# Performance work log

Hardware: AMD Instinct MI355X
Metric: run time of the kernel (lower is better)

Reference implementation:

```python
import jax, jax.numpy as jnp
import numpy as np

B, S, D, H, M = 2, 2048, 1024, 16, 4096  # batch, seqlen, dim, n_heads, max_seq_len
HD = D // H  # head_dim = 64
EPS = 1e-5


def layernorm(x, g, b):
    mu = jnp.mean(x, axis=-1, keepdims=True)
    var = jnp.mean((x - mu) ** 2, axis=-1, keepdims=True)
    return (x - mu) * jax.lax.rsqrt(var + EPS) * g + b


def setup_inputs() -> dict:
    key = jax.random.key(0)
    ks = jax.random.split(key, 5)
    x = jax.random.normal(ks[0], (B, S, D), jnp.float32)
    # causal mask: >=0 -> keep, negative -> drop (forward does att *= mask >= 0)
    i = jnp.arange(S)
    mask = jnp.where(i[None, :] <= i[:, None], 0, -1).astype(jnp.int32)[None, None]
    w1 = jax.random.normal(ks[1], (4 * D, D), jnp.float32) * (D ** -0.5)
    b1 = jnp.zeros((4 * D,), jnp.float32)
    w2 = jax.random.normal(ks[2], (D, D), jnp.float32) * (D ** -0.5)
    b2 = jnp.zeros((D,), jnp.float32)
    g1 = jnp.ones((D,), jnp.float32)
    beta1 = jnp.zeros((D,), jnp.float32)
    g2 = jnp.ones((D,), jnp.float32)
    beta2 = jnp.zeros((D,), jnp.float32)
    pos_w = jax.random.normal(ks[3], (2 * M - 1,), jnp.float32) * 0.02
    return dict(x=x, mask=mask, w1=w1, b1=b1, w2=w2, b2=b2,
                g1=g1, beta1=beta1, g2=g2, beta2=beta2, pos_w=pos_w)


def reference(x, mask, w1, b1, w2, b2, g1, beta1, g2, beta2, pos_w):
    # f1 + silu, split into gate u and q/k/v
    h = jax.nn.silu(x @ w1.T + b1)                      # [B,S,4D]
    u, q, k, v = jnp.split(h, 4, axis=-1)
    to_heads = lambda t: t.reshape(B, S, H, HD).transpose(0, 2, 1, 3)  # [B,H,S,HD]
    u, q, k, v = map(to_heads, (u, q, k, v))
    # relative positional bias: bias[i,j] = pos_w[M-1 + (j - i)]
    rel = jnp.arange(S)[None, :] - jnp.arange(S)[:, None]
    bias = pos_w[M - 1 + rel]                           # [S,S]
    att = jax.nn.silu(jnp.einsum('bhqd,bhkd->bhqk', q, k) + bias)
    att = att * (mask >= 0)                             # [B,H,S,S]
    y = jnp.einsum('bhqk,bhkd->bhqd', att, v) * u
    y = y.transpose(0, 2, 1, 3).reshape(B, S, D)
    y = layernorm(y, g1, beta1)
    y = y @ w2.T + b2
    return layernorm(y + x, g2, beta2)
```

## Files before the change

### kernel.cpp

```cpp
#include <hip/hip_runtime.h>
#include <hip/hip_bf16.h>

#define BN   2
#define SEQ  2048
#define DIM  1024
#define NH   16
#define HD   64
#define D4   4096
#define MAXS 4096

using bf16 = __hip_bfloat16;
typedef __bf16 bf16x8 __attribute__((ext_vector_type(8)));
typedef float  f32x4  __attribute__((ext_vector_type(4)));

__device__ __forceinline__ float bf2f(bf16 v){ return __bfloat162float(v); }
__device__ __forceinline__ bf16  f2bf(float v){ return __float2bfloat16(v); }
__device__ __forceinline__ float silu_f(float v){
  const float e = __expf(-v);
  return v * __builtin_amdgcn_rcpf(1.f + e);
}

__device__ __forceinline__ void async16(void* lds, const void* g){
  __builtin_amdgcn_global_load_lds((const __attribute__((address_space(1))) void*)g,
                                   (__attribute__((address_space(3))) void*)lds, 16, 0, 0);
}
__device__ __forceinline__ f32x4 mfma16(bf16x8 a, bf16x8 b, f32x4 c){
  return __builtin_amdgcn_mfma_f32_16x16x32_bf16(a, b, c, 0, 0, 0);
}

__global__ __launch_bounds__(256) void f2bk3(
    const float* __restrict__ a, bf16* __restrict__ ao, int na,
    const float* __restrict__ b, bf16* __restrict__ bo, int nb,
    const float* __restrict__ c, bf16* __restrict__ co)
{
  int i = (blockIdx.x * 256 + threadIdx.x) * 4;
  const float* in; bf16* out;
  if (i < na){ in = a; out = ao; }
  else if (i < na + nb){ in = b; out = bo; i -= na; }
  else { in = c; out = co; i -= na + nb; }
  const float4 v = *(const float4*)(in + i);
  bf16 t0 = f2bf(v.x), t1 = f2bf(v.y), t2 = f2bf(v.z), t3 = f2bf(v.w);
  ushort4 o;
  o.x = *(unsigned short*)&t0; o.y = *(unsigned short*)&t1;
  o.z = *(unsigned short*)&t2; o.w = *(unsigned short*)&t3;
  *(ushort4*)((unsigned short*)out + i) = o;
}

template<int NTOT>
__global__ __launch_bounds__(256) void gemm_bt(
    const bf16* __restrict__ A, const bf16* __restrict__ W,
    const float* __restrict__ bias, bf16* __restrict__ outb, bf16* __restrict__ vt)
{
  constexpr int K = DIM;
  const int ntiles = NTOT / 128;
  const int m0 = (int)(blockIdx.x / ntiles) * 128;
  const int n0 = (int)(blockIdx.x % ntiles) * 128;
  __shared__ bf16 Al[128*32];
  __shared__ bf16 Bl[128*32];
  const int tid = threadIdx.x, wave = tid>>6, lane = tid&63;
  const int quad = lane>>4, l16 = lane&15;
  const int srow = lane>>2;
  const int sg   = ((lane&3) ^ ((lane>>3)&3)) * 8;
  const int wm = (wave>>1)*64, wn = (wave&1)*64;
  const int rkey = ((l16>>1)&3);

  f32x4 acc[4][4];
  #pragma unroll
  for (int i=0;i<4;i++)
    #pragma unroll
    for (int j=0;j<4;j++) acc[i][j] = (f32x4){0.f,0.f,0.f,0.f};

  const bf16* aB = A + m0*K;
  const bf16* wB = W + n0*K;

  for (int k0 = 0; k0 < K; k0 += 32){
    async16(&Al[wave*1024      ], aB + (wave*32      + srow)*K + k0 + sg);
    async16(&Al[wave*1024 + 512], aB + (wave*32 + 16 + srow)*K + k0 + sg);
    async16(&Bl[wave*1024      ], wB + (wave*32      + srow)*K + k0 + sg);
    async16(&Bl[wave*1024 + 512], wB + (wave*32 + 16 + srow)*K + k0 + sg);
    __syncthreads();
    bf16x8 af[4], bv[4];
    #pragma unroll
    for (int mt=0;mt<4;mt++) af[mt] = *(const bf16x8*)&Al[(wm+mt*16+l16)*32 + (quad ^ rkey)*8];
    #pragma unroll
    for (int nt=0;nt<4;nt++) bv[nt] = *(const bf16x8*)&Bl[(wn+nt*16+l16)*32 + (quad ^ rkey)*8];
    #pragma unroll
    for (int mt=0;mt<4;mt++)
      #pragma unroll
      for (int nt=0;nt<4;nt++)
        acc[mt][nt] = mfma16(af[mt], bv[nt], acc[mt][nt]);
    __syncthreads();
  }

  const bool vtile = (NTOT == 4096) && (n0 >= 3*DIM);
  if (!vtile){
    #pragma unroll
    for (int mt=0;mt<4;mt++){
      #pragma unroll
      for (int nt=0;nt<4;nt++){
        const int row = m0 + wm + mt*16 + quad*4;
        const int col = n0 + wn + nt*16 + l16;
        const float bvv = bias[col];
        #pragma unroll
        for (int r=0;r<4;r++){
          float v = silu_f(acc[mt][nt][r] + bvv);
          outb[(row+r)*NTOT + col] = f2bf(v);
        }
      }
    }
  } else {
    #pragma unroll
    for (int mt=0;mt<4;mt++){
      #pragma unroll
      for (int nt=0;nt<4;nt++){
        const int row = m0 + wm + mt*16 + quad*4;
        const int colg = n0 + wn + nt*16 + l16;
        const float bvv = bias[colg];
        const int col = colg - 3*DIM;
        const int hh = col >> 6, d = col & 63;
        const int bb = row >> 11, sl = row & 2047;
        ushort4 o;
        float v0 = silu_f(acc[mt][nt][0] + bvv);
        float v1 = silu_f(acc[mt][nt][1] + bvv);
        float v2 = silu_f(acc[mt][nt][2] + bvv);
        float v3 = silu_f(acc[mt][nt][3] + bvv);
        bf16 t0=f2bf(v0), t1=f2bf(v1), t2=f2bf(v2), t3=f2bf(v3);
        o.x=*(unsigned short*)&t0; o.y=*(unsigned short*)&t1;
        o.z=*(unsigned short*)&t2; o.w=*(unsigned short*)&t3;
        *(ushort4*)&vt[((bb*NH + hh)*HD + d)*SEQ + sl] = o;
      }
    }
  }
}

__global__ __launch_bounds__(256) void gemm_bt2(
    const bf16* __restrict__ A, const bf16* __restrict__ W,
    const float* __restrict__ bias, const float* __restrict__ resid,
    float* __restrict__ outf)
{
  constexpr int K = DIM, NTOT = DIM;
  const int ntiles = NTOT / 64;
  const int m0 = (int)(blockIdx.x / ntiles) * 128;
  const int n0 = (int)(blockIdx.x % ntiles) * 64;
  __shared__ bf16 Al[128*32];
  __shared__ bf16 Bl[64*32];
  const int tid = threadIdx.x, wave = tid>>6, lane = tid&63;
  const int quad = lane>>4, l16 = lane&15;
  const int srow = lane>>2;
  const int sg   = ((lane&3) ^ ((lane>>3)&3)) * 8;
  const int wm = wave*32;
  const int rkey = ((l16>>1)&3);

  f32x4 acc[2][4];
  #pragma unroll
  for (int i=0;i<2;i++)
    #pragma unroll
    for (int j=0;j<4;j++) acc[i][j] = (f32x4){0.f,0.f,0.f,0.f};

  const bf16* aB = A + m0*K;
  const bf16* wB = W + n0*K;

  for (int k0 = 0; k0 < K; k0 += 32){
    async16(&Al[wave*1024      ], aB + (wave*32      + srow)*K + k0 + sg);
    async16(&Al[wave*1024 + 512], aB + (wave*32 + 16 + srow)*K + k0 + sg);
    async16(&Bl[wave*512       ], wB + (wave*16      + srow)*K + k0 + sg);
    __syncthreads();
    bf16x8 af[2], bv[4];
    #pragma unroll
    for (int mt=0;mt<2;mt++) af[mt] = *(const bf16x8*)&Al[(wm+mt*16+l16)*32 + (quad ^ rkey)*8];
    #pragma unroll
    for (int nt=0;nt<4;nt++) bv[nt] = *(const bf16x8*)&Bl[(nt*16+l16)*32 + (quad ^ rkey)*8];
    #pragma unroll
    for (int mt=0;mt<2;mt++)
      #pragma unroll
      for (int nt=0;nt<4;nt++)
        acc[mt][nt] = mfma16(af[mt], bv[nt], acc[mt][nt]);
    __syncthreads();
  }

  #pragma unroll
  for (int mt=0;mt<2;mt++){
    #pragma unroll
    for (int nt=0;nt<4;nt++){
      const int row = m0 + wm + mt*16 + quad*4;
      const int col = n0 + nt*16 + l16;
      const float bvv = bias[col];
      #pragma unroll
      for (int r=0;r<4;r++){
        outf[(row+r)*NTOT + col] = acc[mt][nt][r] + bvv + resid[(row+r)*NTOT + col];
      }
    }
  }
}

__global__ __launch_bounds__(256) void attn(
    const bf16* __restrict__ h, const bf16* __restrict__ vt,
    const float* __restrict__ pw, bf16* __restrict__ y)
{
  const int bid = blockIdx.x;
  const int g  = (bid & 7) + ((bid >> 7) << 3);
  const int qp = (bid >> 3) & 15;
  const int hh = g & 15, b = g >> 4;
  __shared__ bf16 Kl[128*64];
  __shared__ bf16 Vl[64*128];
  __shared__ bf16 Pl[4][16*136];
  __shared__ float pwl[256];
  const int tid = threadIdx.x, wave = tid>>6, lane = tid&63;
  const int quad = lane>>4, l16 = lane&15;

  const bf16* kgb = h + b*SEQ*D4 + 2*DIM + hh*HD;
  const bf16* vgb = vt + (b*NH + hh)*HD*SEQ;
  const int krow8 = lane>>3;
  const int kgo   = ((lane&7) ^ krow8) * 8;
  const int vrow4 = lane>>4;

  #pragma unroll
  for (int pass = 0; pass < 2; ++pass){
    const int qt = pass ? (31 - qp) : qp;
    const int q0 = qt * 64;

    const bf16* qbase = h + (b*SEQ + q0 + wave*16 + l16)*D4 + DIM + hh*HD;
    bf16x8 qf[2];
    qf[0] = *(const bf16x8*)(qbase + quad*8);
    qf[1] = *(const bf16x8*)(qbase + 32 + quad*8);

    f32x4 oacc[4];
    #pragma unroll
    for (int nt=0;nt<4;nt++) oacc[nt] = (f32x4){0.f,0.f,0.f,0.f};

    const int kmax = q0 + 64;

    bf16x8 kreg[4], vreg[4];
    float pv;
    #pragma unroll
    for (int t=0;t<4;t++)
      kreg[t] = *(const bf16x8*)(kgb + (wave*32 + t*8 + krow8)*D4 + kgo);
    #pragma unroll
    for (int t=0;t<4;t++){
      const int vg = ((lane&15) ^ (t*4 + vrow4)) * 8;
      vreg[t] = *(const bf16x8*)(vgb + (wave*16 + t*4 + vrow4)*SEQ + vg);
    }
    pv = pw[MAXS - 1 - q0 - 63 + tid];

    for (int k0 = 0; k0 < kmax; k0 += 128){
      __syncthreads();
      #pragma unroll
      for (int t=0;t<4;t++)
        *(bf16x8*)&Kl[(wave*32 + t*8)*64 + lane*8] = kreg[t];
      #pragma unroll
      for (int t=0;t<4;t++)
        *(bf16x8*)&Vl[(wave*16 + t*4)*128 + lane*8] = vreg[t];
      pwl[tid] = pv;
      __syncthreads();

      if (k0 + 128 < kmax){
        const int kn = k0 + 128;
        #pragma unroll
        for (int t=0;t<4;t++)
          kreg[t] = *(const bf16x8*)(kgb + (kn + wave*32 + t*8 + krow8)*D4 + kgo);
        #pragma unroll
        for (int t=0;t<4;t++){
          const int vg = ((lane&15) ^ (t*4 + vrow4)) * 8;
          vreg[t] = *(const bf16x8*)(vgb + (wave*16 + t*4 + vrow4)*SEQ + kn + vg);
        }
        pv = pw[MAXS - 1 + kn - q0 - 63 + tid];
      }

      f32x4 sacc[8];
      #pragma unroll
      for (int nt=0;nt<8;nt++) sacc[nt] = (f32x4){0.f,0.f,0.f,0.f};
      __builtin_amdgcn_s_setprio(1);
      #pragma unroll
      for (int ks=0;ks<2;ks++){
        #pragma unroll
        for (int nt=0;nt<8;nt++){
          bf16x8 kf = *(const bf16x8*)&Kl[(nt*16 + l16)*64 + ((ks*4 + quad) ^ (l16&7))*8];
          sacc[nt] = mfma16(kf, qf[ks], sacc[nt]);
        }
      }
      __builtin_amdgcn_s_setprio(0);

      const int dq = q0 - k0;
      const int qrl = wave*16 + l16;
      #pragma unroll
      for (int nt=0;nt<8;nt++){
        const int kb = nt*16 + quad*4;
        ushort4 o;
        bf16 tb[4];
        #pragma unroll
        for (int r=0;r<4;r++){
          const int d = kb + r - qrl;
          const float bias = pwl[d + 63];
          const float sv = silu_f(sacc[nt][r] + bias);
          tb[r] = f2bf((d <= dq) ? sv : 0.f);
        }
        o.x=*(unsigned short*)&tb[0]; o.y=*(unsigned short*)&tb[1];
        o.z=*(unsigned short*)&tb[2]; o.w=*(unsigned short*)&tb[3];
        *(ushort4*)&Pl[wave][l16*136 + kb] = o;
      }

      __builtin_amdgcn_s_setprio(1);
      #pragma unroll
      for (int ks=0;ks<4;ks++){
        bf16x8 pf = *(const bf16x8*)&Pl[wave][l16*136 + ks*32 + quad*8];
        #pragma unroll
        for (int nt=0;nt<4;nt++){
          bf16x8 vf = *(const bf16x8*)&Vl[(nt*16 + l16)*128 + ((ks*4 + quad) ^ l16)*8];
          oacc[nt] = mfma16(pf, vf, oacc[nt]);
        }
      }
      __builtin_amdgcn_s_setprio(0);
    }

    const int qrow = q0 + wave*16 + quad*4;
    #pragma unroll
    for (int nt=0;nt<4;nt++){
      const int c = hh*HD + nt*16 + l16;
      #pragma unroll
      for (int r=0;r<4;r++){
        const int srow = b*SEQ + qrow + r;
        const float uu = bf2f(h[srow*D4 + c]);
        y[srow*DIM + c] = f2bf(oacc[nt][r] * uu);
      }
    }
    __syncthreads();
  }
}


template<bool FP32IN, bool FP32OUT>
__global__ __launch_bounds__(256) void lnorm(const void* __restrict__ in,
    const float* __restrict__ g, const float* __restrict__ be, void* __restrict__ out)
{
  const int row = blockIdx.x;
  const int tid = threadIdx.x, wave = tid>>6, lane = tid&63;
  const int c0 = tid*4;
  float v[4];
  if (FP32IN){
    const float* p = (const float*)in + row*DIM + c0;
    #pragma unroll
    for (int j=0;j<4;j++) v[j] = p[j];
  } else {
    const bf16* p = (const bf16*)in + row*DIM + c0;
    #pragma unroll
    for (int j=0;j<4;j++) v[j] = bf2f(p[j]);
  }
  float s = 0.f, ss = 0.f;
  #pragma unroll
  for (int j=0;j<4;j++){ s += v[j]; ss += v[j]*v[j]; }
  #pragma unroll
  for (int off=32; off>0; off>>=1){
    s  += __shfl_down(s, off);
    ss += __shfl_down(ss, off);
  }
  __shared__ float red[8];
  if (lane==0){ red[wave] = s; red[4+wave] = ss; }
  __syncthreads();
  s  = red[0]+red[1]+red[2]+red[3];
  ss = red[4]+red[5]+red[6]+red[7];
  const float mu   = s * (1.f/DIM);
  const float var  = ss * (1.f/DIM) - mu*mu;
  const float rstd = rsqrtf(var + 1e-5f);
  #pragma unroll
  for (int j=0;j<4;j++){
    const int c = c0 + j;
    const float o = (v[j]-mu)*rstd*g[c] + be[c];
    if (FP32OUT) ((float*)out)[row*DIM + c] = o;
    else         ((bf16*)out)[row*DIM + c] = f2bf(o);
  }
}

extern "C" void kernel_launch(void* const* d_in, const int* in_sizes, int n_in,
                              void* d_out, int out_size, void* d_ws, size_t ws_size,
                              hipStream_t stream)
{
  const float* x   = (const float*)d_in[0];
  const float* w1  = (const float*)d_in[2];
  const float* b1  = (const float*)d_in[3];
  const float* w2  = (const float*)d_in[4];
  const float* b2  = (const float*)d_in[5];
  const float* g1  = (const float*)d_in[6];
  const float* be1 = (const float*)d_in[7];
  const float* g2  = (const float*)d_in[8];
  const float* be2 = (const float*)d_in[9];
  const float* pw  = (const float*)d_in[10];

  char* ws = (char*)d_ws;
  bf16*  h   = (bf16*)(ws);
  bf16*  vt  = (bf16*)(ws + (32u<<20));
  bf16*  y   = (bf16*)(ws + (40u<<20));
  bf16*  xb  = (bf16*)(ws + (48u<<20));
  bf16*  w1b = (bf16*)(ws + (56u<<20));
  bf16*  w2b = (bf16*)(ws + (64u<<20));
  bf16*  l1  = (bf16*)(ws + (66u<<20));
  float* z   = (float*)(ws + (74u<<20));

  const int NX  = BN*SEQ*DIM;
  const int NW1 = 4*DIM*DIM;
  const int NW2 = DIM*DIM;
  f2bk3<<<dim3((NX+NW1+NW2)/1024), dim3(256), 0, stream>>>(x, xb, NX, w1, w1b, NW1, w2, w2b);

  gemm_bt<4096><<<dim3(1024), dim3(256), 0, stream>>>(xb, w1b, b1, h, vt);
  attn<<<dim3(512), dim3(256), 0, stream>>>(h, vt, pw, y);
  lnorm<false,false><<<dim3(4096), dim3(256), 0, stream>>>(y, g1, be1, l1);
  gemm_bt2<<<dim3(512), dim3(256), 0, stream>>>(l1, w2b, b2, x, z);
  lnorm<true,true><<<dim3(4096), dim3(256), 0, stream>>>(z, g2, be2, d_out);
}
```

Baseline: 241.7 us.

## Split attention into one query tile per block, alias P over K in LDS

The attention kernel now launches 1024 blocks with one 64-row query tile each, replacing 512 blocks that each handled a balanced pair of tiles. Block order is reversed so the heaviest causal tiles start first. The P scratch buffer now shares LDS with the K tile, separated by an extra barrier, which shrinks LDS use so launch_bounds can ask for 4 blocks per CU. Tiles lying fully below the diagonal skip the mask select. The cost is an extra sync per k-step and reliance on the hardware scheduler to balance the uneven per-block work.

```diff
diff --git a/kernel.cpp b/kernel.cpp
--- a/kernel.cpp
+++ b/kernel.cpp
@@ -193,18 +193,21 @@
   }
 }
 
-__global__ __launch_bounds__(256) void attn(
+__global__ __launch_bounds__(256, 4) void attn(
     const bf16* __restrict__ h, const bf16* __restrict__ vt,
     const float* __restrict__ pw, bf16* __restrict__ y)
 {
   const int bid = blockIdx.x;
-  const int g  = (bid & 7) + ((bid >> 7) << 3);
-  const int qp = (bid >> 3) & 15;
+  const int g  = (bid & 7) + ((bid >> 8) << 3);
+  const int qt = 31 - ((bid >> 3) & 31);
   const int hh = g & 15, b = g >> 4;
-  __shared__ bf16 Kl[128*64];
-  __shared__ bf16 Vl[64*128];
-  __shared__ bf16 Pl[4][16*136];
-  __shared__ float pwl[256];
+
+  __shared__ __align__(16) char smem[17408 + 16384 + 1024];
+  bf16*  Kl  = (bf16*)smem;
+  bf16*  Pl  = (bf16*)smem;
+  bf16*  Vl  = (bf16*)(smem + 17408);
+  float* pwl = (float*)(smem + 17408 + 16384);
+
   const int tid = threadIdx.x, wave = tid>>6, lane = tid&63;
   const int quad = lane>>4, l16 = lane&15;
 
@@ -214,79 +217,93 @@
   const int kgo   = ((lane&7) ^ krow8) * 8;
   const int vrow4 = lane>>4;
 
-  #pragma unroll
-  for (int pass = 0; pass < 2; ++pass){
-    const int qt = pass ? (31 - qp) : qp;
-    const int q0 = qt * 64;
-
-    const bf16* qbase = h + (b*SEQ + q0 + wave*16 + l16)*D4 + DIM + hh*HD;
-    bf16x8 qf[2];
-    qf[0] = *(const bf16x8*)(qbase + quad*8);
-    qf[1] = *(const bf16x8*)(qbase + 32 + quad*8);
-
-    f32x4 oacc[4];
-    #pragma unroll
-    for (int nt=0;nt<4;nt++) oacc[nt] = (f32x4){0.f,0.f,0.f,0.f};
-
-    const int kmax = q0 + 64;
-
-    bf16x8 kreg[4], vreg[4];
-    float pv;
+  const int q0 = qt * 64;
+
+  const bf16* qbase = h + (b*SEQ + q0 + wave*16 + l16)*D4 + DIM + hh*HD;
+  bf16x8 qf[2];
+  qf[0] = *(const bf16x8*)(qbase + quad*8);
+  qf[1] = *(const bf16x8*)(qbase + 32 + quad*8);
+
+  f32x4 oacc[4];
+  #pragma unroll
+  for (int nt=0;nt<4;nt++) oacc[nt] = (f32x4){0.f,0.f,0.f,0.f};
+
+  const int kmax = q0 + 64;
+
+  bf16x8 kreg[4], vreg[4];
+  float pv;
+  #pragma unroll
+  for (int t=0;t<4;t++)
+    kreg[t] = *(const bf16x8*)(kgb + (wave*32 + t*8 + krow8)*D4 + kgo);
+  #pragma unroll
+  for (int t=0;t<4;t++){
+    const int vg = ((lane&15) ^ (t*4 + vrow4)) * 8;
+    vreg[t] = *(const bf16x8*)(vgb + (wave*16 + t*4 + vrow4)*SEQ + vg);
+  }
+  pv = pw[MAXS - 1 - q0 - 63 + tid];
+
+  for (int k0 = 0; k0 < kmax; k0 += 128){
+    __syncthreads();
     #pragma unroll
     for (int t=0;t<4;t++)
-      kreg[t] = *(const bf16x8*)(kgb + (wave*32 + t*8 + krow8)*D4 + kgo);
-    #pragma unroll
-    for (int t=0;t<4;t++){
-      const int vg = ((lane&15) ^ (t*4 + vrow4)) * 8;
-      vreg[t] = *(const bf16x8*)(vgb + (wave*16 + t*4 + vrow4)*SEQ + vg);
-    }
-    pv = pw[MAXS - 1 - q0 - 63 + tid];
-
-    for (int k0 = 0; k0 < kmax; k0 += 128){
-      __syncthreads();
+      *(bf16x8*)&Kl[(wave*32 + t*8)*64 + lane*8] = kreg[t];
+    #pragma unroll
+    for (int t=0;t<4;t++)
+      *(bf16x8*)&Vl[(wave*16 + t*4)*128 + lane*8] = vreg[t];
+    pwl[tid] = pv;
+    __syncthreads();
+
+    if (k0 + 128 < kmax){
+      const int kn = k0 + 128;
       #pragma unroll
       for (int t=0;t<4;t++)
-        *(bf16x8*)&Kl[(wave*32 + t*8)*64 + lane*8] = kreg[t];
-      #pragma unroll
-      for (int t=0;t<4;t++)
-        *(bf16x8*)&Vl[(wave*16 + t*4)*128 + lane*8] = vreg[t];
-      pwl[tid] = pv;
-      __syncthreads();
-
-      if (k0 + 128 < kmax){
-        const int kn = k0 + 128;
-        #pragma unroll
-        for (int t=0;t<4;t++)
-          kreg[t] = *(const bf16x8*)(kgb + (kn + wave*32 + t*8 + krow8)*D4 + kgo);
-        #pragma unroll
-        for (int t=0;t<4;t++){
-          const int vg = ((lane&15) ^ (t*4 + vrow4)) * 8;
-          vreg[t] = *(const bf16x8*)(vgb + (wave*16 + t*4 + vrow4)*SEQ + kn + vg);
-        }
-        pv = pw[MAXS - 1 + kn - q0 - 63 + tid];
-      }
-
-      f32x4 sacc[8];
-      #pragma unroll
-      for (int nt=0;nt<8;nt++) sacc[nt] = (f32x4){0.f,0.f,0.f,0.f};
-      __builtin_amdgcn_s_setprio(1);
-      #pragma unroll
-      for (int ks=0;ks<2;ks++){
-        #pragma unroll
-        for (int nt=0;nt<8;nt++){
-          bf16x8 kf = *(const bf16x8*)&Kl[(nt*16 + l16)*64 + ((ks*4 + quad) ^ (l16&7))*8];
-          sacc[nt] = mfma16(kf, qf[ks], sacc[nt]);
-        }
-      }
-      __builtin_amdgcn_s_setprio(0);
-
-      const int dq = q0 - k0;
-      const int qrl = wave*16 + l16;
+        kreg[t] = *(const bf16x8*)(kgb + (kn + wave*32 + t*8 + krow8)*D4 + kgo);
+      #pragma unroll
+      for (int t=0;t<4;t++){
+        const int vg = ((lane&15) ^ (t*4 + vrow4)) * 8;
+        vreg[t] = *(const bf16x8*)(vgb + (wave*16 + t*4 + vrow4)*SEQ + kn + vg);
+      }
+      pv = pw[MAXS - 1 + kn - q0 - 63 + tid];
+    }
+
+    f32x4 sacc[8];
+    #pragma unroll
+    for (int nt=0;nt<8;nt++) sacc[nt] = (f32x4){0.f,0.f,0.f,0.f};
+    __builtin_amdgcn_s_setprio(1);
+    #pragma unroll
+    for (int ks=0;ks<2;ks++){
+      #pragma unroll
+      for (int nt=0;nt<8;nt++){
+        bf16x8 kf = *(const bf16x8*)&Kl[(nt*16 + l16)*64 + ((ks*4 + quad) ^ (l16&7))*8];
+        sacc[nt] = mfma16(kf, qf[ks], sacc[nt]);
+      }
+    }
+    __builtin_amdgcn_s_setprio(0);
+    __syncthreads();
+
+    bf16* Plw = Pl + wave*(16*136);
+    const int dq = q0 - k0;
+    const int qrl = wave*16 + l16;
+    if (dq >= 127){
       #pragma unroll
       for (int nt=0;nt<8;nt++){
         const int kb = nt*16 + quad*4;
-        ushort4 o;
-        bf16 tb[4];
+        ushort4 o; bf16 tb[4];
+        #pragma unroll
+        for (int r=0;r<4;r++){
+          const int d = kb + r - qrl;
+          const float bias = pwl[d + 63];
+          tb[r] = f2bf(silu_f(sacc[nt][r] + bias));
+        }
+        o.x=*(unsigned short*)&tb[0]; o.y=*(unsigned short*)&tb[1];
+        o.z=*(unsigned short*)&tb[2]; o.w=*(unsigned short*)&tb[3];
+        *(ushort4*)&Plw[l16*136 + kb] = o;
+      }
+    } else {
+      #pragma unroll
+      for (int nt=0;nt<8;nt++){
+        const int kb = nt*16 + quad*4;
+        ushort4 o; bf16 tb[4];
         #pragma unroll
         for (int r=0;r<4;r++){
           const int d = kb + r - qrl;
@@ -296,34 +313,33 @@
         }
         o.x=*(unsigned short*)&tb[0]; o.y=*(unsigned short*)&tb[1];
         o.z=*(unsigned short*)&tb[2]; o.w=*(unsigned short*)&tb[3];
-        *(ushort4*)&Pl[wave][l16*136 + kb] = o;
-      }
-
-      __builtin_amdgcn_s_setprio(1);
-      #pragma unroll
-      for (int ks=0;ks<4;ks++){
-        bf16x8 pf = *(const bf16x8*)&Pl[wave][l16*136 + ks*32 + quad*8];
-        #pragma unroll
-        for (int nt=0;nt<4;nt++){
-          bf16x8 vf = *(const bf16x8*)&Vl[(nt*16 + l16)*128 + ((ks*4 + quad) ^ l16)*8];
-          oacc[nt] = mfma16(pf, vf, oacc[nt]);
-        }
-      }
-      __builtin_amdgcn_s_setprio(0);
-    }
-
-    const int qrow = q0 + wave*16 + quad*4;
-    #pragma unroll
-    for (int nt=0;nt<4;nt++){
-      const int c = hh*HD + nt*16 + l16;
-      #pragma unroll
-      for (int r=0;r<4;r++){
-        const int srow = b*SEQ + qrow + r;
-        const float uu = bf2f(h[srow*D4 + c]);
-        y[srow*DIM + c] = f2bf(oacc[nt][r] * uu);
-      }
-    }
-    __syncthreads();
+        *(ushort4*)&Plw[l16*136 + kb] = o;
+      }
+    }
+
+    __builtin_amdgcn_s_setprio(1);
+    #pragma unroll
+    for (int ks=0;ks<4;ks++){
+      bf16x8 pf = *(const bf16x8*)&Plw[l16*136 + ks*32 + quad*8];
+      #pragma unroll
+      for (int nt=0;nt<4;nt++){
+        bf16x8 vf = *(const bf16x8*)&Vl[(nt*16 + l16)*128 + ((ks*4 + quad) ^ l16)*8];
+        oacc[nt] = mfma16(pf, vf, oacc[nt]);
+      }
+    }
+    __builtin_amdgcn_s_setprio(0);
+  }
+
+  const int qrow = q0 + wave*16 + quad*4;
+  #pragma unroll
+  for (int nt=0;nt<4;nt++){
+    const int c = hh*HD + nt*16 + l16;
+    #pragma unroll
+    for (int r=0;r<4;r++){
+      const int srow = b*SEQ + qrow + r;
+      const float uu = bf2f(h[srow*D4 + c]);
+      y[srow*DIM + c] = f2bf(oacc[nt][r] * uu);
+    }
   }
 }
 
@@ -401,7 +417,7 @@
   f2bk3<<<dim3((NX+NW1+NW2)/1024), dim3(256), 0, stream>>>(x, xb, NX, w1, w1b, NW1, w2, w2b);
 
   gemm_bt<4096><<<dim3(1024), dim3(256), 0, stream>>>(xb, w1b, b1, h, vt);
-  attn<<<dim3(512), dim3(256), 0, stream>>>(h, vt, pw, y);
+  attn<<<dim3(1024), dim3(256), 0, stream>>>(h, vt, pw, y);
   lnorm<false,false><<<dim3(4096), dim3(256), 0, stream>>>(y, g1, be1, l1);
   gemm_bt2<<<dim3(512), dim3(256), 0, stream>>>(l1, w2b, b2, x, z);
   lnorm<true,true><<<dim3(4096), dim3(256), 0, stream>>>(z, g2, be2, d_out);
```

After: 310.2 us. 28.4% more time.
